# Optimization experiments

Measured on AMD Instinct MI355X. Metric: run time of the kernel, lower is better.

Reference implementation:

```python
import jax, jax.numpy as jnp
import numpy as np

K_IN = 9      # input_patch_size
K_OUT = 3     # output_patch_size
C_IN = 4      # nb_of_input_features
C_OUT = 2     # nb_of_output_features
HID = 50      # int_layer_width
B, H, W = 16, 128, 128
CUT = K_IN // 2 - K_OUT // 2  # border pixels cut from output (3)


def _unfold(x, k):
    # x: [B, C, H, W] -> [B, C*k*k, L] with torch unfold ordering (c, ki, kj)
    b, c, h, w = x.shape
    ho, wo = h - k + 1, w - k + 1
    cols = jnp.stack([x[:, :, i:i + ho, j:j + wo]
                      for i in range(k) for j in range(k)], axis=2)  # [B,C,k*k,ho,wo]
    return cols.reshape(b, c * k * k, ho * wo)


def _fold_add(patches, oh, ow):
    # patches: [B, C, k, k, ho, wo] -> overlap-add into [B, C, oh, ow]
    b, c, k, _, ho, wo = patches.shape
    out = jnp.zeros((b, c, oh, ow), dtype=patches.dtype)
    for i in range(k):
        for j in range(k):
            out = out.at[:, :, i:i + ho, j:j + wo].add(patches[:, :, i, j])
    return out


def setup_inputs() -> dict:
    key = jax.random.key(0)
    ks = jax.random.split(key, 7)
    f_in = C_IN * K_IN * K_IN      # 324
    f_out = C_OUT * K_OUT * K_OUT  # 18
    s1 = 1.0 / np.sqrt(f_in)
    s2 = 1.0 / np.sqrt(HID)
    return {
        "x": jax.random.normal(ks[0], (B, C_IN, H, W), dtype=jnp.float32),
        "W1": jax.random.uniform(ks[1], (f_in, HID), jnp.float32, -s1, s1),
        "b1": jax.random.uniform(ks[2], (HID,), jnp.float32, -s1, s1),
        "W2": jax.random.uniform(ks[3], (HID, HID), jnp.float32, -s2, s2),
        "b2": jax.random.uniform(ks[4], (HID,), jnp.float32, -s2, s2),
        "W3": jax.random.uniform(ks[5], (HID, f_out), jnp.float32, -s2, s2),
        "b3": jax.random.uniform(ks[6], (f_out,), jnp.float32, -s2, s2),
    }


def reference(x, W1, b1, W2, b2, W3, b3):
    b, c, h, w = x.shape
    oh, ow = h - 2 * CUT, w - 2 * CUT          # 122, 122
    ho, wo = h - K_IN + 1, w - K_IN + 1        # 120, 120 (= oh-K_OUT+1)
    # unfold -> [B, L, C_in*K_in^2] -> flatten rows
    cols = _unfold(x, K_IN)                    # [B, 324, L]
    feats = cols.transpose(0, 2, 1).reshape(b * ho * wo, -1)
    # 3-layer MLP
    hmid = jax.nn.relu(feats @ W1 + b1)
    hmid = jax.nn.relu(hmid @ W2 + b2)
    out = hmid @ W3 + b3                       # [B*L, C_out*K_out^2]
    # fold (overlap-add), torch feature ordering (c, ki, kj)
    patches = out.reshape(b, ho, wo, C_OUT, K_OUT, K_OUT)
    patches = patches.transpose(0, 3, 4, 5, 1, 2)  # [B, C_out, k, k, ho, wo]
    res = _fold_add(patches, oh, ow)
    # divisor = fold(unfold(ones)) -> per-pixel overlap count
    ones_patches = jnp.ones((1, 1, K_OUT, K_OUT, ho, wo), dtype=x.dtype)
    divisor = _fold_add(ones_patches, oh, ow)  # [1,1,oh,ow]
    return res / divisor
```

## Files before the change

### kernel.cpp

```cpp
#include <hip/hip_runtime.h>
#include <hip/hip_bf16.h>

#define BATCH   16
#define C_INF   4
#define H_IN    128
#define W_IN    128
#define HID     50
#define F_OUT   18
#define HO      120
#define WO      120
#define OH      122
#define OW      122
#define NPOS    (BATCH * HO * WO)
#define MBLK    128
#define NBLKS   (NPOS / MBLK)
#define NXCD    8

#define NB1     (11*4*64*8)
#define NB2     (2*4*64*8)
#define NB3     (2*2*64*8)
#define NWF     (NB1 + NB2 + NB3)
#define WOFF    (NPOS * F_OUT)
#define NXC     (BATCH * C_INF * H_IN * W_IN)
#define PREP_BLOCKS  ((NWF + 255) / 256)
#define XCONV_BLOCKS (NXC / (256 * 8))
#define CW      16

typedef float    v4f     __attribute__((ext_vector_type(4)));
typedef short    short4v __attribute__((ext_vector_type(4)));
typedef short    short8  __attribute__((ext_vector_type(8)));
typedef _Float16 v8hf    __attribute__((ext_vector_type(8)));
typedef int      v4i     __attribute__((ext_vector_type(4)));
typedef short8 short8_a4 __attribute__((aligned(4)));

__device__ inline short f2h(float x) {
    _Float16 h = (_Float16)x;
    return __builtin_bit_cast(short, h);
}
__device__ inline float h2f(short s) {
    return (float)__builtin_bit_cast(_Float16, s);
}
__device__ inline void keepv(short8 x) {
    asm volatile("" :: "v"(__builtin_bit_cast(v4i, x)));
}
__device__ inline void keepi(v4i x) {
    asm volatile("" :: "v"(x));
}

__device__ inline int hswz(int m, int j) {
    return (m * 64 + j) ^ ((m & 7) << 3);
}

__device__ inline int slot_to_k1(int s, int qb, int e) {
    if (s < 9) {
        int pair = s*4 + qb;
        int c = pair/9, ki = pair - c*9;
        return c*81 + ki*9 + e;
    }
    int r = (s-9)*32 + qb*8 + e;
    if (r >= 36) return -1;
    int c = r/9, ki = r - c*9;
    return c*81 + ki*9 + 8;
}

__global__ __launch_bounds__(256)
void prep_kernel(const float* __restrict__ x,
                 const float* __restrict__ W1, const float* __restrict__ W2,
                 const float* __restrict__ W3, short* __restrict__ wf,
                 short* __restrict__ xe, short* __restrict__ xo)
{
    const int blk = blockIdx.x;
    if (blk >= PREP_BLOCKS) {
        const int j = ((blk - PREP_BLOCKS)*256 + (int)threadIdx.x) * 8;
        v4f a = *(const v4f*)&x[j];
        v4f b = *(const v4f*)&x[j + 4];
        float c9 = (j + 8 < NXC) ? x[j + 8] : 0.f;
        short s[9];
        #pragma unroll
        for (int e = 0; e < 4; ++e) { s[e] = f2h(a[e]); s[e+4] = f2h(b[e]); }
        s[8] = f2h(c9);
        short8 ve, vo;
        #pragma unroll
        for (int e = 0; e < 8; ++e) { ve[e] = s[e]; vo[e] = s[e+1]; }
        *(short8*)&xe[j] = ve;
        *(short8*)&xo[j] = vo;
        return;
    }
    int i = blk * 256 + threadIdx.x;
    if (i >= NWF) return;
    float val;
    if (i < NB1) {
        int t = i;
        int e = t & 7, lane = (t >> 3) & 63;
        int rest = t >> 9;
        int u = rest & 3, s = rest >> 2;
        int k = slot_to_k1(s, lane >> 4, e);
        int n = u*16 + (lane & 15);
        val = (k >= 0 && n < HID) ? W1[k*HID + n] : 0.f;
    } else if (i < NB1 + NB2) {
        int t = i - NB1;
        int e = t & 7, lane = (t >> 3) & 63;
        int rest = t >> 9;
        int u = rest & 3, s = rest >> 2;
        int k = s*32 + ((lane >> 4) << 3) + e;
        int n = u*16 + (lane & 15);
        val = (k < HID && n < HID) ? W2[k*HID + n] : 0.f;
    } else {
        int t = i - NB1 - NB2;
        int e = t & 7, lane = (t >> 3) & 63;
        int rest = t >> 9;
        int u = rest & 1, s = rest >> 1;
        int k = s*32 + ((lane >> 4) << 3) + e;
        int n = u*16 + (lane & 15);
        val = (k < HID && n < F_OUT) ? W3[k*F_OUT + n] : 0.f;
    }
    wf[i] = f2h(val);
}

__global__ __launch_bounds__(256, 2)
void mfma_mlp(const short* __restrict__ xe, const short* __restrict__ xo,
              const float* __restrict__ b1, const float* __restrict__ b2,
              const float* __restrict__ b3,
              const short* __restrict__ wf, short* __restrict__ out3)
{
    __shared__ short wlds[NB1];
    __shared__ short h_lds[128 * 64];

    const int tid  = threadIdx.x;
    const int lane = tid & 63;
    const int w    = tid >> 6;
    const int q    = lane >> 4, col = lane & 15;
    const int swz   = (blockIdx.x & 7) * (NBLKS / NXCD) + (blockIdx.x >> 3);
    const int mbase = swz * MBLK;
    const int mw    = w * 32;

    const short* xp[2];
    #pragma unroll
    for (int t = 0; t < 2; ++t) {
        int pos = mbase + mw + t*16 + col;
        int b   = pos / (HO*WO); int rem = pos - b*(HO*WO);
        int y   = rem / WO;      int xc  = rem - y*WO;
        int bi  = b*(C_INF*H_IN*W_IN) + y*W_IN + xc;
        xp[t] = (bi & 1) ? (xo + (bi - 1)) : (xe + bi);
    }

    short8 ah[9][2];
    #pragma unroll
    for (int s = 0; s < 9; ++s) {
        const int pair = s*4 + q;
        const int c = pair/9, ki = pair - c*9;
        const int off = c*(H_IN*W_IN) + ki*W_IN;
        #pragma unroll
        for (int t = 0; t < 2; ++t)
            ah[s][t] = *(const short8_a4*)(xp[t] + off);
    }
    short8 ahr[2][2];
    #pragma unroll
    for (int sr = 0; sr < 2; ++sr) {
        #pragma unroll
        for (int e = 0; e < 8; ++e) {
            int r = sr*32 + q*8 + e;
            bool valid = (r < 36);
            int c = valid ? r/9 : 0;
            int ki = r - c*9;
            int off = c*(H_IN*W_IN) + ki*W_IN + 8;
            #pragma unroll
            for (int t = 0; t < 2; ++t)
                ahr[sr][t][e] = valid ? xp[t][off] : (short)0;
        }
    }

    #pragma unroll
    for (int it = 0; it < 11; ++it) {
        const int cbase = it*256 + w*64;
        const short* g  = wf + (cbase + lane)*8;
        __builtin_amdgcn_global_load_lds(
            (const __attribute__((address_space(1))) void*)g,
            (__attribute__((address_space(3))) void*)&wlds[cbase*8],
            16, 0, 0);
    }

    float bias1[4], bias2[4], bias3[2];
    #pragma unroll
    for (int u = 0; u < 4; ++u) {
        int j = u*16 + col;
        bias1[u] = (j < HID) ? b1[j] : 0.f;
        bias2[u] = (j < HID) ? b2[j] : 0.f;
    }
    #pragma unroll
    for (int u = 0; u < 2; ++u) {
        int j = u*16 + col;
        bias3[u] = (j < F_OUT) ? b3[j] : 0.f;
    }

    const v4i* B2L = (const v4i*)(wf + NB1) + lane;
    const v4i* B3L = (const v4i*)(wf + NB1 + NB2) + lane;

    #pragma unroll
    for (int s = 0; s < 9; ++s) { keepv(ah[s][0]); keepv(ah[s][1]); }
    #pragma unroll
    for (int sr = 0; sr < 2; ++sr) { keepv(ahr[sr][0]); keepv(ahr[sr][1]); }

    __syncthreads();

    v4f acc[2][4];
    #pragma unroll
    for (int t = 0; t < 2; ++t)
        #pragma unroll
        for (int u = 0; u < 4; ++u)
            acc[t][u] = (v4f){0.f, 0.f, 0.f, 0.f};

    #pragma unroll
    for (int s = 0; s < 9; ++s) {
        #pragma unroll
        for (int u = 0; u < 4; ++u) {
            v4i bv = *(const v4i*)&wlds[((s*4 + u)*64 + lane)*8];
            v8hf bh = __builtin_bit_cast(v8hf, bv);
            #pragma unroll
            for (int t = 0; t < 2; ++t) {
                v8hf a_h = __builtin_bit_cast(v8hf, ah[s][t]);
                acc[t][u] = __builtin_amdgcn_mfma_f32_16x16x32_f16(a_h, bh, acc[t][u], 0, 0, 0);
            }
        }
    }
    #pragma unroll
    for (int sr = 0; sr < 2; ++sr) {
        const int s = 9 + sr;
        #pragma unroll
        for (int u = 0; u < 4; ++u) {
            v4i bv = *(const v4i*)&wlds[((s*4 + u)*64 + lane)*8];
            v8hf bh = __builtin_bit_cast(v8hf, bv);
            #pragma unroll
            for (int t = 0; t < 2; ++t) {
                v8hf a_h = __builtin_bit_cast(v8hf, ahr[sr][t]);
                acc[t][u] = __builtin_amdgcn_mfma_f32_16x16x32_f16(a_h, bh, acc[t][u], 0, 0, 0);
            }
        }
    }

    v4i b2r[8], b3r[4];
    #pragma unroll
    for (int i = 0; i < 8; ++i) b2r[i] = B2L[i*64];
    #pragma unroll
    for (int i = 0; i < 4; ++i) b3r[i] = B3L[i*64];
    #pragma unroll
    for (int i = 0; i < 8; ++i) keepi(b2r[i]);
    #pragma unroll
    for (int i = 0; i < 4; ++i) keepi(b3r[i]);

    #pragma unroll
    for (int u = 0; u < 4; ++u) {
        #pragma unroll
        for (int t = 0; t < 2; ++t) {
            #pragma unroll
            for (int r = 0; r < 4; ++r) {
                float v = fmaxf(acc[t][u][r] + bias1[u], 0.f);
                int m = mw + t*16 + q*4 + r;
                h_lds[hswz(m, u*16 + col)] = f2h(v);
            }
        }
    }

    v4f acc2[2][4];
    #pragma unroll
    for (int t = 0; t < 2; ++t)
        #pragma unroll
        for (int u = 0; u < 4; ++u)
            acc2[t][u] = (v4f){0.f, 0.f, 0.f, 0.f};

    #pragma unroll
    for (int s = 0; s < 2; ++s) {
        short8 ah2[2];
        #pragma unroll
        for (int t = 0; t < 2; ++t) {
            int m = mw + t*16 + col;
            ah2[t] = *(const short8*)&h_lds[hswz(m, s*32 + q*8)];
        }
        #pragma unroll
        for (int u = 0; u < 4; ++u) {
            v8hf bh = __builtin_bit_cast(v8hf, b2r[s*4 + u]);
            #pragma unroll
            for (int t = 0; t < 2; ++t) {
                v8hf a_h = __builtin_bit_cast(v8hf, ah2[t]);
                acc2[t][u] = __builtin_amdgcn_mfma_f32_16x16x32_f16(a_h, bh, acc2[t][u], 0, 0, 0);
            }
        }
    }

    #pragma unroll
    for (int u = 0; u < 4; ++u) {
        #pragma unroll
        for (int t = 0; t < 2; ++t) {
            #pragma unroll
            for (int r = 0; r < 4; ++r) {
                float v = fmaxf(acc2[t][u][r] + bias2[u], 0.f);
                int m = mw + t*16 + q*4 + r;
                h_lds[hswz(m, u*16 + col)] = f2h(v);
            }
        }
    }

    v4f acc3[2][2];
    #pragma unroll
    for (int t = 0; t < 2; ++t)
        #pragma unroll
        for (int u = 0; u < 2; ++u)
            acc3[t][u] = (v4f){0.f, 0.f, 0.f, 0.f};

    #pragma unroll
    for (int s = 0; s < 2; ++s) {
        short8 ah3[2];
        #pragma unroll
        for (int t = 0; t < 2; ++t) {
            int m = mw + t*16 + col;
            ah3[t] = *(const short8*)&h_lds[hswz(m, s*32 + q*8)];
        }
        #pragma unroll
        for (int u = 0; u < 2; ++u) {
            v8hf bh = __builtin_bit_cast(v8hf, b3r[s*2 + u]);
            #pragma unroll
            for (int t = 0; t < 2; ++t) {
                v8hf a_h = __builtin_bit_cast(v8hf, ah3[t]);
                acc3[t][u] = __builtin_amdgcn_mfma_f32_16x16x32_f16(a_h, bh, acc3[t][u], 0, 0, 0);
            }
        }
    }

    #pragma unroll
    for (int u = 0; u < 2; ++u) {
        int j = u*16 + col;
        if (j < F_OUT) {
            #pragma unroll
            for (int t = 0; t < 2; ++t) {
                short4v vs;
                #pragma unroll
                for (int r = 0; r < 4; ++r) vs[r] = f2h(acc3[t][u][r] + bias3[u]);
                __builtin_nontemporal_store(vs,
                    (short4v*)&out3[j*NPOS + mbase + mw + t*16 + q*4]);
            }
        }
    }
}

__global__ __launch_bounds__(256)
void fold_kernel(const short* __restrict__ out3, float* __restrict__ out)
{
    const int idx = blockIdx.x * 256 + threadIdx.x;
    const int total = BATCH * 2 * OH * CW;
    if (idx >= total) return;

    int t = idx;
    const int cx = t % CW; t /= CW;
    const int oy = t % OH; t /= OH;
    const int c  = t & 1;  t >>= 1;
    const int b  = t;
    const int ox0 = cx * 8;

    if (oy >= 2 && oy < HO && cx >= 1 && cx <= 14) {
        float accv[8];
        #pragma unroll
        for (int e = 0; e < 8; ++e) accv[e] = 0.f;
        #pragma unroll
        for (int ki = 0; ki < 3; ++ki) {
            const int y    = oy - ki;
            const int rowb = (b*HO + y)*WO;
            const int ob   = (c*3 + ki)*3;
            short8 v0 = *(const short8_a4*)&out3[(ob + 0)*NPOS + rowb + ox0];
            short8 v1 = *(const short8_a4*)&out3[(ob + 1)*NPOS + rowb + ox0 - 2];
            int   v1b = *(const int*)      &out3[(ob + 1)*NPOS + rowb + ox0 + 6];
            short8 v2 = *(const short8_a4*)&out3[(ob + 2)*NPOS + rowb + ox0 - 2];
            #pragma unroll
            for (int e = 0; e < 8; ++e) {
                accv[e] += h2f(v0[e]);
                accv[e] += (e < 7) ? h2f(v1[e + 1]) : h2f((short)(v1b & 0xffff));
                accv[e] += h2f(v2[e]);
            }
        }
        float* op = &out[((b*2 + c)*OH + oy)*OW + ox0];
        #pragma unroll
        for (int e = 0; e < 8; ++e) op[e] = accv[e] / 9.f;
        return;
    }

    #pragma unroll
    for (int e = 0; e < 8; ++e) {
        const int ox = ox0 + e;
        if (ox < OW) {
            const int ylo = max(0, oy - 2), yhi = min(HO - 1, oy);
            const int xlo = max(0, ox - 2), xhi = min(WO - 1, ox);
            float s = 0.f;
            for (int y = ylo; y <= yhi; ++y) {
                const int ki = oy - y;
                for (int xx = xlo; xx <= xhi; ++xx) {
                    const int kj = ox - xx;
                    const int o  = (c*3 + ki)*3 + kj;
                    s += h2f(out3[o*NPOS + (b*HO + y)*WO + xx]);
                }
            }
            const float div = (float)((yhi - ylo + 1) * (xhi - xlo + 1));
            out[((b*2 + c)*OH + oy)*OW + ox] = s / div;
        }
    }
}

extern "C" void kernel_launch(void* const* d_in, const int* in_sizes, int n_in,
                              void* d_out, int out_size, void* d_ws, size_t ws_size,
                              hipStream_t stream)
{
    const float* x  = (const float*)d_in[0];
    const float* W1 = (const float*)d_in[1];
    const float* b1 = (const float*)d_in[2];
    const float* W2 = (const float*)d_in[3];
    const float* b2 = (const float*)d_in[4];
    const float* W3 = (const float*)d_in[5];
    const float* b3 = (const float*)d_in[6];

    short* out3 = (short*)d_ws;
    short* wf   = out3 + WOFF;
    short* xe   = wf + NWF;
    short* xo   = xe + NXC;

    prep_kernel<<<PREP_BLOCKS + XCONV_BLOCKS, 256, 0, stream>>>(x, W1, W2, W3, wf, xe, xo);

    mfma_mlp<<<NBLKS, 256, 0, stream>>>(xe, xo, b1, b2, b3, wf, out3);

    const int total = BATCH * 2 * OH * CW;
    fold_kernel<<<(total + 255) / 256, 256, 0, stream>>>(out3, (float*)d_out);
}
```

Before: 116.6 us.

## Make MLP kernel persistent with next-chunk input prefetch and smaller weight LDS

Converts the MLP kernel from one block per 128-position chunk into a persistent grid of 768 blocks that loop over chunks. The weight staging into LDS is done once per block, and the next chunk's input patches are loaded from global memory while the current chunk's layer 2/3 work runs. LDS staging shrinks to the first 9 K-slices, with the remainder slices and W2/W3 read directly from global/L2 each iteration, which allows 3 blocks per CU. It trades more register pressure and repeated global weight reads for amortized weight loading and overlap of input loads with compute.

```diff
diff --git a/kernel.cpp b/kernel.cpp
--- a/kernel.cpp
+++ b/kernel.cpp
@@ -13,8 +13,8 @@
 #define OW      122
 #define NPOS    (BATCH * HO * WO)
 #define MBLK    128
-#define NBLKS   (NPOS / MBLK)
-#define NXCD    8
+#define NCH     (NPOS / MBLK)
+#define GBLK    768
 
 #define NB1     (11*4*64*8)
 #define NB2     (2*4*64*8)
@@ -25,6 +25,7 @@
 #define PREP_BLOCKS  ((NWF + 255) / 256)
 #define XCONV_BLOCKS (NXC / (256 * 8))
 #define CW      16
+#define NSTG    (36*512)
 
 typedef float    v4f     __attribute__((ext_vector_type(4)));
 typedef short    short4v __attribute__((ext_vector_type(4)));
@@ -43,12 +44,13 @@
 __device__ inline void keepv(short8 x) {
     asm volatile("" :: "v"(__builtin_bit_cast(v4i, x)));
 }
-__device__ inline void keepi(v4i x) {
-    asm volatile("" :: "v"(x));
-}
 
 __device__ inline int hswz(int m, int j) {
     return (m * 64 + j) ^ ((m & 7) << 3);
+}
+
+__device__ inline int chunk_base(int c) {
+    return (((c & 7) * (NCH / 8)) + (c >> 3)) * MBLK;
 }
 
 __device__ inline int slot_to_k1(int s, int qb, int e) {
@@ -117,61 +119,23 @@
     wf[i] = f2h(val);
 }
 
-__global__ __launch_bounds__(256, 2)
+__global__ __launch_bounds__(256, 3)
 void mfma_mlp(const short* __restrict__ xe, const short* __restrict__ xo,
               const float* __restrict__ b1, const float* __restrict__ b2,
               const float* __restrict__ b3,
               const short* __restrict__ wf, short* __restrict__ out3)
 {
-    __shared__ short wlds[NB1];
+    __shared__ short wlds[NSTG];
     __shared__ short h_lds[128 * 64];
 
     const int tid  = threadIdx.x;
     const int lane = tid & 63;
     const int w    = tid >> 6;
     const int q    = lane >> 4, col = lane & 15;
-    const int swz   = (blockIdx.x & 7) * (NBLKS / NXCD) + (blockIdx.x >> 3);
-    const int mbase = swz * MBLK;
-    const int mw    = w * 32;
-
-    const short* xp[2];
+    const int mw   = w * 32;
+
     #pragma unroll
-    for (int t = 0; t < 2; ++t) {
-        int pos = mbase + mw + t*16 + col;
-        int b   = pos / (HO*WO); int rem = pos - b*(HO*WO);
-        int y   = rem / WO;      int xc  = rem - y*WO;
-        int bi  = b*(C_INF*H_IN*W_IN) + y*W_IN + xc;
-        xp[t] = (bi & 1) ? (xo + (bi - 1)) : (xe + bi);
-    }
-
-    short8 ah[9][2];
-    #pragma unroll
-    for (int s = 0; s < 9; ++s) {
-        const int pair = s*4 + q;
-        const int c = pair/9, ki = pair - c*9;
-        const int off = c*(H_IN*W_IN) + ki*W_IN;
-        #pragma unroll
-        for (int t = 0; t < 2; ++t)
-            ah[s][t] = *(const short8_a4*)(xp[t] + off);
-    }
-    short8 ahr[2][2];
-    #pragma unroll
-    for (int sr = 0; sr < 2; ++sr) {
-        #pragma unroll
-        for (int e = 0; e < 8; ++e) {
-            int r = sr*32 + q*8 + e;
-            bool valid = (r < 36);
-            int c = valid ? r/9 : 0;
-            int ki = r - c*9;
-            int off = c*(H_IN*W_IN) + ki*W_IN + 8;
-            #pragma unroll
-            for (int t = 0; t < 2; ++t)
-                ahr[sr][t][e] = valid ? xp[t][off] : (short)0;
-        }
-    }
-
-    #pragma unroll
-    for (int it = 0; it < 11; ++it) {
+    for (int it = 0; it < 9; ++it) {
         const int cbase = it*256 + w*64;
         const short* g  = wf + (cbase + lane)*8;
         __builtin_amdgcn_global_load_lds(
@@ -193,152 +157,227 @@
         bias3[u] = (j < F_OUT) ? b3[j] : 0.f;
     }
 
+    const v4i* B1L = (const v4i*)wf + lane;
     const v4i* B2L = (const v4i*)(wf + NB1) + lane;
     const v4i* B3L = (const v4i*)(wf + NB1 + NB2) + lane;
 
-    #pragma unroll
-    for (int s = 0; s < 9; ++s) { keepv(ah[s][0]); keepv(ah[s][1]); }
-    #pragma unroll
-    for (int sr = 0; sr < 2; ++sr) { keepv(ahr[sr][0]); keepv(ahr[sr][1]); }
+    int ch = blockIdx.x;
+    int mb = chunk_base(ch);
+    const short* xp[2];
+    short8 ah[9][2], ahr[2][2];
+    {
+        #pragma unroll
+        for (int t = 0; t < 2; ++t) {
+            int pos = mb + mw + t*16 + col;
+            int b   = pos / (HO*WO); int rem = pos - b*(HO*WO);
+            int y   = rem / WO;      int xc  = rem - y*WO;
+            int bi  = b*(C_INF*H_IN*W_IN) + y*W_IN + xc;
+            xp[t] = (bi & 1) ? (xo + (bi - 1)) : (xe + bi);
+        }
+        #pragma unroll
+        for (int s = 0; s < 9; ++s) {
+            const int pair = s*4 + q;
+            const int c = pair/9, ki = pair - c*9;
+            const int off = c*(H_IN*W_IN) + ki*W_IN;
+            #pragma unroll
+            for (int t = 0; t < 2; ++t)
+                ah[s][t] = *(const short8_a4*)(xp[t] + off);
+        }
+        #pragma unroll
+        for (int sr = 0; sr < 2; ++sr) {
+            #pragma unroll
+            for (int e = 0; e < 8; ++e) {
+                int r = sr*32 + q*8 + e;
+                bool valid = (r < 36);
+                int c = valid ? r/9 : 0;
+                int ki = r - c*9;
+                int off = c*(H_IN*W_IN) + ki*W_IN + 8;
+                #pragma unroll
+                for (int t = 0; t < 2; ++t)
+                    ahr[sr][t][e] = valid ? xp[t][off] : (short)0;
+            }
+        }
+        #pragma unroll
+        for (int s = 0; s < 9; ++s) { keepv(ah[s][0]); keepv(ah[s][1]); }
+        #pragma unroll
+        for (int sr = 0; sr < 2; ++sr) { keepv(ahr[sr][0]); keepv(ahr[sr][1]); }
+    }
 
     __syncthreads();
 
-    v4f acc[2][4];
-    #pragma unroll
-    for (int t = 0; t < 2; ++t)
-        #pragma unroll
-        for (int u = 0; u < 4; ++u)
-            acc[t][u] = (v4f){0.f, 0.f, 0.f, 0.f};
-
-    #pragma unroll
-    for (int s = 0; s < 9; ++s) {
+    #pragma unroll 1
+    for (;;) {
+        v4f acc[2][4];
+        #pragma unroll
+        for (int t = 0; t < 2; ++t)
+            #pragma unroll
+            for (int u = 0; u < 4; ++u)
+                acc[t][u] = (v4f){0.f, 0.f, 0.f, 0.f};
+
+        #pragma unroll
+        for (int s = 0; s < 9; ++s) {
+            #pragma unroll
+            for (int u = 0; u < 4; ++u) {
+                v4i bv = *(const v4i*)&wlds[((s*4 + u)*64 + lane)*8];
+                v8hf bh = __builtin_bit_cast(v8hf, bv);
+                #pragma unroll
+                for (int t = 0; t < 2; ++t) {
+                    v8hf a_h = __builtin_bit_cast(v8hf, ah[s][t]);
+                    acc[t][u] = __builtin_amdgcn_mfma_f32_16x16x32_f16(a_h, bh, acc[t][u], 0, 0, 0);
+                }
+            }
+        }
+        #pragma unroll
+        for (int sr = 0; sr < 2; ++sr) {
+            const int s = 9 + sr;
+            #pragma unroll
+            for (int u = 0; u < 4; ++u) {
+                v8hf bh = __builtin_bit_cast(v8hf, B1L[(s*4 + u)*64]);
+                #pragma unroll
+                for (int t = 0; t < 2; ++t) {
+                    v8hf a_h = __builtin_bit_cast(v8hf, ahr[sr][t]);
+                    acc[t][u] = __builtin_amdgcn_mfma_f32_16x16x32_f16(a_h, bh, acc[t][u], 0, 0, 0);
+                }
+            }
+        }
+
+        const int nxt  = ch + GBLK;
+        const bool more = (nxt < NCH);
+        if (more) {
+            int mbn = chunk_base(nxt);
+            #pragma unroll
+            for (int t = 0; t < 2; ++t) {
+                int pos = mbn + mw + t*16 + col;
+                int b   = pos / (HO*WO); int rem = pos - b*(HO*WO);
+                int y   = rem / WO;      int xc  = rem - y*WO;
+                int bi  = b*(C_INF*H_IN*W_IN) + y*W_IN + xc;
+                xp[t] = (bi & 1) ? (xo + (bi - 1)) : (xe + bi);
+            }
+            #pragma unroll
+            for (int s = 0; s < 9; ++s) {
+                const int pair = s*4 + q;
+                const int c = pair/9, ki = pair - c*9;
+                const int off = c*(H_IN*W_IN) + ki*W_IN;
+                #pragma unroll
+                for (int t = 0; t < 2; ++t)
+                    ah[s][t] = *(const short8_a4*)(xp[t] + off);
+            }
+            #pragma unroll
+            for (int sr = 0; sr < 2; ++sr) {
+                #pragma unroll
+                for (int e = 0; e < 8; ++e) {
+                    int r = sr*32 + q*8 + e;
+                    bool valid = (r < 36);
+                    int c = valid ? r/9 : 0;
+                    int ki = r - c*9;
+                    int off = c*(H_IN*W_IN) + ki*W_IN + 8;
+                    #pragma unroll
+                    for (int t = 0; t < 2; ++t)
+                        ahr[sr][t][e] = valid ? xp[t][off] : (short)0;
+                }
+            }
+        }
+
         #pragma unroll
         for (int u = 0; u < 4; ++u) {
-            v4i bv = *(const v4i*)&wlds[((s*4 + u)*64 + lane)*8];
-            v8hf bh = __builtin_bit_cast(v8hf, bv);
             #pragma unroll
             for (int t = 0; t < 2; ++t) {
-                v8hf a_h = __builtin_bit_cast(v8hf, ah[s][t]);
-                acc[t][u] = __builtin_amdgcn_mfma_f32_16x16x32_f16(a_h, bh, acc[t][u], 0, 0, 0);
-            }
-        }
-    }
-    #pragma unroll
-    for (int sr = 0; sr < 2; ++sr) {
-        const int s = 9 + sr;
+                #pragma unroll
+                for (int r = 0; r < 4; ++r) {
+                    float v = fmaxf(acc[t][u][r] + bias1[u], 0.f);
+                    int m = mw + t*16 + q*4 + r;
+                    h_lds[hswz(m, u*16 + col)] = f2h(v);
+                }
+            }
+        }
+
+        v4f acc2[2][4];
+        #pragma unroll
+        for (int t = 0; t < 2; ++t)
+            #pragma unroll
+            for (int u = 0; u < 4; ++u)
+                acc2[t][u] = (v4f){0.f, 0.f, 0.f, 0.f};
+
+        #pragma unroll
+        for (int s = 0; s < 2; ++s) {
+            short8 ah2[2];
+            #pragma unroll
+            for (int t = 0; t < 2; ++t) {
+                int m = mw + t*16 + col;
+                ah2[t] = *(const short8*)&h_lds[hswz(m, s*32 + q*8)];
+            }
+            #pragma unroll
+            for (int u = 0; u < 4; ++u) {
+                v8hf bh = __builtin_bit_cast(v8hf, B2L[(s*4 + u)*64]);
+                #pragma unroll
+                for (int t = 0; t < 2; ++t) {
+                    v8hf a_h = __builtin_bit_cast(v8hf, ah2[t]);
+                    acc2[t][u] = __builtin_amdgcn_mfma_f32_16x16x32_f16(a_h, bh, acc2[t][u], 0, 0, 0);
+                }
+            }
+        }
+
         #pragma unroll
         for (int u = 0; u < 4; ++u) {
-            v4i bv = *(const v4i*)&wlds[((s*4 + u)*64 + lane)*8];
-            v8hf bh = __builtin_bit_cast(v8hf, bv);
             #pragma unroll
             for (int t = 0; t < 2; ++t) {
-                v8hf a_h = __builtin_bit_cast(v8hf, ahr[sr][t]);
-                acc[t][u] = __builtin_amdgcn_mfma_f32_16x16x32_f16(a_h, bh, acc[t][u], 0, 0, 0);
-            }
-        }
-    }
-
-    v4i b2r[8], b3r[4];
-    #pragma unroll
-    for (int i = 0; i < 8; ++i) b2r[i] = B2L[i*64];
-    #pragma unroll
-    for (int i = 0; i < 4; ++i) b3r[i] = B3L[i*64];
-    #pragma unroll
-    for (int i = 0; i < 8; ++i) keepi(b2r[i]);
-    #pragma unroll
-    for (int i = 0; i < 4; ++i) keepi(b3r[i]);
-
-    #pragma unroll
-    for (int u = 0; u < 4; ++u) {
-        #pragma unroll
-        for (int t = 0; t < 2; ++t) {
-            #pragma unroll
-            for (int r = 0; r < 4; ++r) {
-                float v = fmaxf(acc[t][u][r] + bias1[u], 0.f);
-                int m = mw + t*16 + q*4 + r;
-                h_lds[hswz(m, u*16 + col)] = f2h(v);
-            }
-        }
-    }
-
-    v4f acc2[2][4];
-    #pragma unroll
-    for (int t = 0; t < 2; ++t)
-        #pragma unroll
-        for (int u = 0; u < 4; ++u)
-            acc2[t][u] = (v4f){0.f, 0.f, 0.f, 0.f};
-
-    #pragma unroll
-    for (int s = 0; s < 2; ++s) {
-        short8 ah2[2];
-        #pragma unroll
-        for (int t = 0; t < 2; ++t) {
-            int m = mw + t*16 + col;
-            ah2[t] = *(const short8*)&h_lds[hswz(m, s*32 + q*8)];
-        }
-        #pragma unroll
-        for (int u = 0; u < 4; ++u) {
-            v8hf bh = __builtin_bit_cast(v8hf, b2r[s*4 + u]);
+                #pragma unroll
+                for (int r = 0; r < 4; ++r) {
+                    float v = fmaxf(acc2[t][u][r] + bias2[u], 0.f);
+                    int m = mw + t*16 + q*4 + r;
+                    h_lds[hswz(m, u*16 + col)] = f2h(v);
+                }
+            }
+        }
+
+        v4f acc3[2][2];
+        #pragma unroll
+        for (int t = 0; t < 2; ++t)
+            #pragma unroll
+            for (int u = 0; u < 2; ++u)
+                acc3[t][u] = (v4f){0.f, 0.f, 0.f, 0.f};
+
+        #pragma unroll
+        for (int s = 0; s < 2; ++s) {
+            short8 ah3[2];
             #pragma unroll
             for (int t = 0; t < 2; ++t) {
-                v8hf a_h = __builtin_bit_cast(v8hf, ah2[t]);
-                acc2[t][u] = __builtin_amdgcn_mfma_f32_16x16x32_f16(a_h, bh, acc2[t][u], 0, 0, 0);
-            }
-        }
-    }
-
-    #pragma unroll
-    for (int u = 0; u < 4; ++u) {
-        #pragma unroll
-        for (int t = 0; t < 2; ++t) {
-            #pragma unroll
-            for (int r = 0; r < 4; ++r) {
-                float v = fmaxf(acc2[t][u][r] + bias2[u], 0.f);
-                int m = mw + t*16 + q*4 + r;
-                h_lds[hswz(m, u*16 + col)] = f2h(v);
-            }
-        }
-    }
-
-    v4f acc3[2][2];
-    #pragma unroll
-    for (int t = 0; t < 2; ++t)
-        #pragma unroll
-        for (int u = 0; u < 2; ++u)
-            acc3[t][u] = (v4f){0.f, 0.f, 0.f, 0.f};
-
-    #pragma unroll
-    for (int s = 0; s < 2; ++s) {
-        short8 ah3[2];
-        #pragma unroll
-        for (int t = 0; t < 2; ++t) {
-            int m = mw + t*16 + col;
-            ah3[t] = *(const short8*)&h_lds[hswz(m, s*32 + q*8)];
-        }
+                int m = mw + t*16 + col;
+                ah3[t] = *(const short8*)&h_lds[hswz(m, s*32 + q*8)];
+            }
+            #pragma unroll
+            for (int u = 0; u < 2; ++u) {
+                v8hf bh = __builtin_bit_cast(v8hf, B3L[(s*2 + u)*64]);
+                #pragma unroll
+                for (int t = 0; t < 2; ++t) {
+                    v8hf a_h = __builtin_bit_cast(v8hf, ah3[t]);
+                    acc3[t][u] = __builtin_amdgcn_mfma_f32_16x16x32_f16(a_h, bh, acc3[t][u], 0, 0, 0);
+                }
+            }
+        }
+
         #pragma unroll
         for (int u = 0; u < 2; ++u) {
-            v8hf bh = __builtin_bit_cast(v8hf, b3r[s*2 + u]);
-            #pragma unroll
-            for (int t = 0; t < 2; ++t) {
-                v8hf a_h = __builtin_bit_cast(v8hf, ah3[t]);
-                acc3[t][u] = __builtin_amdgcn_mfma_f32_16x16x32_f16(a_h, bh, acc3[t][u], 0, 0, 0);
-            }
-        }
-    }
-
-    #pragma unroll
-    for (int u = 0; u < 2; ++u) {
-        int j = u*16 + col;
-        if (j < F_OUT) {
-            #pragma unroll
-            for (int t = 0; t < 2; ++t) {
-                short4v vs;
-                #pragma unroll
-                for (int r = 0; r < 4; ++r) vs[r] = f2h(acc3[t][u][r] + bias3[u]);
-                __builtin_nontemporal_store(vs,
-                    (short4v*)&out3[j*NPOS + mbase + mw + t*16 + q*4]);
-            }
-        }
+            int j = u*16 + col;
+            if (j < F_OUT) {
+                #pragma unroll
+                for (int t = 0; t < 2; ++t) {
+                    short4v vs;
+                    #pragma unroll
+                    for (int r = 0; r < 4; ++r) vs[r] = f2h(acc3[t][u][r] + bias3[u]);
+                    __builtin_nontemporal_store(vs,
+                        (short4v*)&out3[j*NPOS + mb + mw + t*16 + q*4]);
+                }
+            }
+        }
+
+        if (!more) break;
+        #pragma unroll
+        for (int s = 0; s < 9; ++s) { keepv(ah[s][0]); keepv(ah[s][1]); }
+        #pragma unroll
+        for (int sr = 0; sr < 2; ++sr) { keepv(ahr[sr][0]); keepv(ahr[sr][1]); }
+        ch = nxt;
+        mb = chunk_base(ch);
     }
 }
 
@@ -422,7 +461,7 @@
 
     prep_kernel<<<PREP_BLOCKS + XCONV_BLOCKS, 256, 0, stream>>>(x, W1, W2, W3, wf, xe, xo);
 
-    mfma_mlp<<<NBLKS, 256, 0, stream>>>(xe, xo, b1, b2, b3, wf, out3);
+    mfma_mlp<<<GBLK, 256, 0, stream>>>(xe, xo, b1, b2, b3, wf, out3);
 
     const int total = BATCH * 2 * OH * CW;
     fold_kernel<<<(total + 255) / 256, 256, 0, stream>>>(out3, (float*)d_out);
```

Result: slower. 159.7 us (+36.9%).

## Shrink W1 LDS staging and raise occupancy to three blocks per CU

Applied to the files above, without the earlier changes.

Only the first 9 of the 11 layer-1 weight chunks are now staged in LDS. The last 8 B-fragments are loaded straight from global memory into registers just before the remainder MFMAs. This cuts per-block LDS use so three blocks can fit per CU, and the launch bounds are raised to 3 to match. Activation and layer-2/3 weight loads become inline-asm global loads with explicit vmcnt drains, giving control over load scheduling. The risks are higher register pressure under the tighter launch bound and extra global traffic for the weights that are no longer staged.

```diff
diff --git a/kernel.cpp b/kernel.cpp
--- a/kernel.cpp
+++ b/kernel.cpp
@@ -25,6 +25,7 @@
 #define PREP_BLOCKS  ((NWF + 255) / 256)
 #define XCONV_BLOCKS (NXC / (256 * 8))
 #define CW      16
+#define NSTG    (36*512)
 
 typedef float    v4f     __attribute__((ext_vector_type(4)));
 typedef short    short4v __attribute__((ext_vector_type(4)));
@@ -40,11 +41,15 @@
 __device__ inline float h2f(short s) {
     return (float)__builtin_bit_cast(_Float16, s);
 }
-__device__ inline void keepv(short8 x) {
-    asm volatile("" :: "v"(__builtin_bit_cast(v4i, x)));
-}
-__device__ inline void keepi(v4i x) {
-    asm volatile("" :: "v"(x));
+
+__device__ inline v4i aload16(const void* p) {
+    v4i r;
+    asm volatile("global_load_dwordx4 %0, %1, off" : "=v"(r) : "v"(p));
+    return r;
+}
+__device__ inline void vm_drain() {
+    asm volatile("s_waitcnt vmcnt(0)" ::: "memory");
+    __builtin_amdgcn_sched_barrier(0);
 }
 
 __device__ inline int hswz(int m, int j) {
@@ -117,13 +122,13 @@
     wf[i] = f2h(val);
 }
 
-__global__ __launch_bounds__(256, 2)
+__global__ __launch_bounds__(256, 3)
 void mfma_mlp(const short* __restrict__ xe, const short* __restrict__ xo,
               const float* __restrict__ b1, const float* __restrict__ b2,
               const float* __restrict__ b3,
               const short* __restrict__ wf, short* __restrict__ out3)
 {
-    __shared__ short wlds[NB1];
+    __shared__ short wlds[NSTG];
     __shared__ short h_lds[128 * 64];
 
     const int tid  = threadIdx.x;
@@ -144,7 +149,7 @@
         xp[t] = (bi & 1) ? (xo + (bi - 1)) : (xe + bi);
     }
 
-    short8 ah[9][2];
+    v4i ahm[9][2];
     #pragma unroll
     for (int s = 0; s < 9; ++s) {
         const int pair = s*4 + q;
@@ -152,8 +157,19 @@
         const int off = c*(H_IN*W_IN) + ki*W_IN;
         #pragma unroll
         for (int t = 0; t < 2; ++t)
-            ah[s][t] = *(const short8_a4*)(xp[t] + off);
-    }
+            ahm[s][t] = aload16(xp[t] + off);
+    }
+
+    #pragma unroll
+    for (int it = 0; it < 9; ++it) {
+        const int cbase = it*256 + w*64;
+        const short* g  = wf + (cbase + lane)*8;
+        __builtin_amdgcn_global_load_lds(
+            (const __attribute__((address_space(1))) void*)g,
+            (__attribute__((address_space(3))) void*)&wlds[cbase*8],
+            16, 0, 0);
+    }
+
     short8 ahr[2][2];
     #pragma unroll
     for (int sr = 0; sr < 2; ++sr) {
@@ -170,16 +186,6 @@
         }
     }
 
-    #pragma unroll
-    for (int it = 0; it < 11; ++it) {
-        const int cbase = it*256 + w*64;
-        const short* g  = wf + (cbase + lane)*8;
-        __builtin_amdgcn_global_load_lds(
-            (const __attribute__((address_space(1))) void*)g,
-            (__attribute__((address_space(3))) void*)&wlds[cbase*8],
-            16, 0, 0);
-    }
-
     float bias1[4], bias2[4], bias3[2];
     #pragma unroll
     for (int u = 0; u < 4; ++u) {
@@ -193,15 +199,12 @@
         bias3[u] = (j < F_OUT) ? b3[j] : 0.f;
     }
 
+    const v4i* B1L = (const v4i*)wf + lane;
     const v4i* B2L = (const v4i*)(wf + NB1) + lane;
     const v4i* B3L = (const v4i*)(wf + NB1 + NB2) + lane;
 
-    #pragma unroll
-    for (int s = 0; s < 9; ++s) { keepv(ah[s][0]); keepv(ah[s][1]); }
-    #pragma unroll
-    for (int sr = 0; sr < 2; ++sr) { keepv(ahr[sr][0]); keepv(ahr[sr][1]); }
-
     __syncthreads();
+    __builtin_amdgcn_sched_barrier(0);
 
     v4f acc[2][4];
     #pragma unroll
@@ -218,18 +221,22 @@
             v8hf bh = __builtin_bit_cast(v8hf, bv);
             #pragma unroll
             for (int t = 0; t < 2; ++t) {
-                v8hf a_h = __builtin_bit_cast(v8hf, ah[s][t]);
+                v8hf a_h = __builtin_bit_cast(v8hf, ahm[s][t]);
                 acc[t][u] = __builtin_amdgcn_mfma_f32_16x16x32_f16(a_h, bh, acc[t][u], 0, 0, 0);
             }
         }
     }
+
+    v4i brem[8];
+    #pragma unroll
+    for (int i = 0; i < 8; ++i) brem[i] = aload16(B1L + (36 + i)*64);
+    vm_drain();
+
     #pragma unroll
     for (int sr = 0; sr < 2; ++sr) {
-        const int s = 9 + sr;
         #pragma unroll
         for (int u = 0; u < 4; ++u) {
-            v4i bv = *(const v4i*)&wlds[((s*4 + u)*64 + lane)*8];
-            v8hf bh = __builtin_bit_cast(v8hf, bv);
+            v8hf bh = __builtin_bit_cast(v8hf, brem[sr*4 + u]);
             #pragma unroll
             for (int t = 0; t < 2; ++t) {
                 v8hf a_h = __builtin_bit_cast(v8hf, ahr[sr][t]);
@@ -240,13 +247,9 @@
 
     v4i b2r[8], b3r[4];
     #pragma unroll
-    for (int i = 0; i < 8; ++i) b2r[i] = B2L[i*64];
-    #pragma unroll
-    for (int i = 0; i < 4; ++i) b3r[i] = B3L[i*64];
-    #pragma unroll
-    for (int i = 0; i < 8; ++i) keepi(b2r[i]);
-    #pragma unroll
-    for (int i = 0; i < 4; ++i) keepi(b3r[i]);
+    for (int i = 0; i < 8; ++i) b2r[i] = aload16(B2L + i*64);
+    #pragma unroll
+    for (int i = 0; i < 4; ++i) b3r[i] = aload16(B3L + i*64);
 
     #pragma unroll
     for (int u = 0; u < 4; ++u) {
@@ -260,6 +263,8 @@
             }
         }
     }
+
+    vm_drain();
 
     v4f acc2[2][4];
     #pragma unroll
```

Measured after the change: 113.8 us. 2.4% less time.
